# Performance work log

Measured on AMD Instinct MI355X. Metric: run time of the kernel, lower is better.

## Reference

```python
import jax, jax.numpy as jnp
import numpy as np

ALPHA = 0.2  # LeakyReLU negative slope
MASK_VAL = -1e12


def setup_inputs() -> dict:
    key = jax.random.key(0)
    k1, k2, k3, k4 = jax.random.split(key, 4)
    B, N, F_in, F_out = 16, 1024, 128, 64
    inp = jax.random.normal(k1, (B, N, F_in), dtype=jnp.float32)
    adj = jax.random.randint(k2, (B, N, N), 0, 2, dtype=jnp.int32)
    W = jax.random.normal(k3, (F_in, F_out), dtype=jnp.float32) * (1.414 / np.sqrt(F_in))
    a = jax.random.normal(k4, (2 * F_out, 1), dtype=jnp.float32) * (1.414 / np.sqrt(2 * F_out))
    return {"inp": inp, "adj": adj, "W": W, "a": a}


def reference(inp, adj, W, a):
    # inp: [B, N, F_in], adj: [B, N, N], W: [F_in, F_out], a: [2*F_out, 1]
    F_out = W.shape[1]
    h = jnp.einsum('bnf,fo->bno', inp, W)  # [B, N, F_out]
    # e_ij = LeakyReLU(a1 . h_i + a2 . h_j)  (equivalent to concat-then-matmul)
    a1 = a[:F_out, 0]  # [F_out]
    a2 = a[F_out:, 0]  # [F_out]
    e = jax.nn.leaky_relu(
        (h @ a1)[:, :, None] + (h @ a2)[:, None, :], negative_slope=ALPHA
    )  # [B, N, N]
    scores = jnp.where(adj > 0, e, MASK_VAL)
    attention = jax.nn.softmax(scores, axis=-1)  # [B, N, N]
    # dropout with p=0.0 / eval mode -> identity
    h_prime = jnp.einsum('bij,bjo->bio', attention, h)  # [B, N, F_out]
    return jax.nn.elu(h_prime)  # concat=True
```

## Files before the change

kernel.cpp:

```cpp
#include <hip/hip_runtime.h>
#include <cstdint>

#define BB   16
#define NN   1024
#define FIN  128
#define FOUT 64
#define ALPHA_S 0.2f

typedef float    f32x4 __attribute__((ext_vector_type(4)));
typedef _Float16 half8 __attribute__((ext_vector_type(8)));

__device__ inline float wave_sum(float v){
  #pragma unroll
  for (int off = 32; off; off >>= 1) v += __shfl_xor(v, off, 64);
  return v;
}

__global__ __launch_bounds__(256) void k_proj(const float* __restrict__ inp,
                                              const float* __restrict__ W,
                                              const float* __restrict__ a,
                                              _Float16* __restrict__ hT_hi,
                                              _Float16* __restrict__ hT_lo,
                                              float* __restrict__ s1,
                                              float* __restrict__ s2){
  __shared__ float inp_s[32 * FIN];
  const int t = threadIdx.x;
  const int w = t >> 6, f = t & 63;
  const int row0 = blockIdx.x * 32;

  {
    const float4* gsrc = (const float4*)(inp + (size_t)row0 * FIN);
    float4* ldst = (float4*)inp_s;
    #pragma unroll
    for (int i = 0; i < 4; ++i) ldst[i * 256 + t] = gsrc[i * 256 + t];
  }
  __syncthreads();

  float acc[8] = {0.f,0.f,0.f,0.f,0.f,0.f,0.f,0.f};
  const float* ls = inp_s + w * 8 * FIN;
  #pragma unroll 4
  for (int k4 = 0; k4 < 32; ++k4){
    float w0 = W[(k4 * 4 + 0) * FOUT + f];
    float w1 = W[(k4 * 4 + 1) * FOUT + f];
    float w2 = W[(k4 * 4 + 2) * FOUT + f];
    float w3 = W[(k4 * 4 + 3) * FOUT + f];
    #pragma unroll
    for (int r = 0; r < 8; ++r){
      float4 iv = *(const float4*)(ls + r * FIN + k4 * 4);
      acc[r] = fmaf(iv.x, w0, acc[r]);
      acc[r] = fmaf(iv.y, w1, acc[r]);
      acc[r] = fmaf(iv.z, w2, acc[r]);
      acc[r] = fmaf(iv.w, w3, acc[r]);
    }
  }

  const float a1f = a[f], a2f = a[FOUT + f];
  const int rbase = row0 + w * 8;
  #pragma unroll
  for (int r = 0; r < 8; ++r){
    float v1 = wave_sum(acc[r] * a1f);
    float v2 = wave_sum(acc[r] * a2f);
    if (f == 0){ s1[rbase + r] = v1; s2[rbase + r] = v2; }
  }

  half8 hv, lv;
  #pragma unroll
  for (int r = 0; r < 8; ++r){
    _Float16 hi = (_Float16)acc[r];
    hv[r] = hi;
    lv[r] = (_Float16)(acc[r] - (float)hi);
  }
  const int b  = row0 >> 10;
  const int j0 = (row0 & 1023) + w * 8;
  size_t idx = (size_t)b * 65536 + (size_t)(j0 >> 5) * 2048
             + (size_t)f * 32 + (size_t)(j0 & 31);
  *(half8*)(hT_hi + idx) = hv;
  *(half8*)(hT_lo + idx) = lv;
}

__global__ __launch_bounds__(256) void k_attn(const int* __restrict__ adj,
                                              const _Float16* __restrict__ hT_hi,
                                              const _Float16* __restrict__ hT_lo,
                                              const float* __restrict__ s1,
                                              const float* __restrict__ s2,
                                              float* __restrict__ out){
  __shared__ float s2_s[NN];
  __shared__ float redmax[4][16];
  __shared__ float redl[4][16];
  __shared__ float csum[4][1088];

  const int t = threadIdx.x;
  const int w = t >> 6, lane = t & 63;
  const int m16 = lane & 15, g = lane >> 4;
  const int b  = blockIdx.x >> 6;
  const int i0 = (blockIdx.x & 63) * 16;
  const int jb = w * 256;

  *(float4*)&s2_s[jb + lane * 4] = *(const float4*)(s2 + b * NN + jb + lane * 4);

  const float s1i = s1[b * NN + i0 + m16];

  const int* arow = adj + ((size_t)(b * NN + i0 + m16)) * NN + jb + g * 8;
  int4 A0[8], A1[8];
  #pragma unroll
  for (int kk = 0; kk < 8; ++kk){
    A0[kk] = *(const int4*)(arow + kk * 32);
    A1[kk] = *(const int4*)(arow + kk * 32 + 4);
  }

  unsigned mask_lo = 0u, mask_hi = 0u;
  float mxp = -3.0e38f;
  #pragma unroll
  for (int kk = 0; kk < 8; ++kk){
    float4 sA = *(const float4*)&s2_s[jb + kk * 32 + g * 8];
    float4 sB = *(const float4*)&s2_s[jb + kk * 32 + g * 8 + 4];
    unsigned bits = 0u;
    bits |= (A0[kk].x > 0) ? 1u   : 0u;  mxp = fmaxf(mxp, A0[kk].x > 0 ? sA.x : -3.0e38f);
    bits |= (A0[kk].y > 0) ? 2u   : 0u;  mxp = fmaxf(mxp, A0[kk].y > 0 ? sA.y : -3.0e38f);
    bits |= (A0[kk].z > 0) ? 4u   : 0u;  mxp = fmaxf(mxp, A0[kk].z > 0 ? sA.z : -3.0e38f);
    bits |= (A0[kk].w > 0) ? 8u   : 0u;  mxp = fmaxf(mxp, A0[kk].w > 0 ? sA.w : -3.0e38f);
    bits |= (A1[kk].x > 0) ? 16u  : 0u;  mxp = fmaxf(mxp, A1[kk].x > 0 ? sB.x : -3.0e38f);
    bits |= (A1[kk].y > 0) ? 32u  : 0u;  mxp = fmaxf(mxp, A1[kk].y > 0 ? sB.y : -3.0e38f);
    bits |= (A1[kk].z > 0) ? 64u  : 0u;  mxp = fmaxf(mxp, A1[kk].z > 0 ? sB.z : -3.0e38f);
    bits |= (A1[kk].w > 0) ? 128u : 0u;  mxp = fmaxf(mxp, A1[kk].w > 0 ? sB.w : -3.0e38f);
    if (kk < 4) mask_lo |= bits << (kk * 8);
    else        mask_hi |= bits << ((kk - 4) * 8);
  }

  mxp = fmaxf(mxp, __shfl_xor(mxp, 16, 64));
  mxp = fmaxf(mxp, __shfl_xor(mxp, 32, 64));
  if (g == 0) redmax[w][m16] = mxp;
  __syncthreads();
  float mxg = fmaxf(fmaxf(redmax[0][m16], redmax[1][m16]),
                    fmaxf(redmax[2][m16], redmax[3][m16]));
  const bool empty = (mxg < -1.0e38f);
  const float xm = s1i + mxg;
  const float mrow = fmaxf(xm, ALPHA_S * xm);

  f32x4 acc0 = {0,0,0,0}, acc1 = {0,0,0,0}, acc2 = {0,0,0,0}, acc3 = {0,0,0,0};
  float psum = 0.f;
  const size_t bbase = (size_t)b * 65536 + (size_t)(w * 8) * 2048
                     + (size_t)m16 * 32 + (size_t)g * 8;
  const _Float16* bhp = hT_hi + bbase;
  const _Float16* blp = hT_lo + bbase;

  #pragma unroll
  for (int kk = 0; kk < 8; ++kk){
    float4 sA = *(const float4*)&s2_s[jb + kk * 32 + g * 8];
    float4 sB = *(const float4*)&s2_s[jb + kk * 32 + g * 8 + 4];
    const unsigned bits = (kk < 4) ? (mask_lo >> (kk * 8)) : (mask_hi >> ((kk - 4) * 8));
    const float sv[8] = {sA.x, sA.y, sA.z, sA.w, sB.x, sB.y, sB.z, sB.w};
    half8 af;
    #pragma unroll
    for (int u = 0; u < 8; ++u){
      float x = s1i + sv[u];
      float e = fmaxf(x, ALPHA_S * x);
      float p = __expf(e - mrow);
      p = ((bits >> u) & 1u) ? p : 0.0f;
      p = empty ? 1.0f : p;
      psum += p;
      af[u] = (_Float16)p;
    }
    half8 b0h = *(const half8*)(bhp + kk * 2048);
    half8 b1h = *(const half8*)(bhp + kk * 2048 + 512);
    half8 b2h = *(const half8*)(bhp + kk * 2048 + 1024);
    half8 b3h = *(const half8*)(bhp + kk * 2048 + 1536);
    half8 b0l = *(const half8*)(blp + kk * 2048);
    half8 b1l = *(const half8*)(blp + kk * 2048 + 512);
    half8 b2l = *(const half8*)(blp + kk * 2048 + 1024);
    half8 b3l = *(const half8*)(blp + kk * 2048 + 1536);
    acc0 = __builtin_amdgcn_mfma_f32_16x16x32_f16(af, b0h, acc0, 0, 0, 0);
    acc0 = __builtin_amdgcn_mfma_f32_16x16x32_f16(af, b0l, acc0, 0, 0, 0);
    acc1 = __builtin_amdgcn_mfma_f32_16x16x32_f16(af, b1h, acc1, 0, 0, 0);
    acc1 = __builtin_amdgcn_mfma_f32_16x16x32_f16(af, b1l, acc1, 0, 0, 0);
    acc2 = __builtin_amdgcn_mfma_f32_16x16x32_f16(af, b2h, acc2, 0, 0, 0);
    acc2 = __builtin_amdgcn_mfma_f32_16x16x32_f16(af, b2l, acc2, 0, 0, 0);
    acc3 = __builtin_amdgcn_mfma_f32_16x16x32_f16(af, b3h, acc3, 0, 0, 0);
    acc3 = __builtin_amdgcn_mfma_f32_16x16x32_f16(af, b3l, acc3, 0, 0, 0);
  }

  psum += __shfl_xor(psum, 16, 64);
  psum += __shfl_xor(psum, 32, 64);
  if (g == 0) redl[w][m16] = psum;

  #pragma unroll
  for (int q = 0; q < 4; ++q){
    csum[w][(g * 4 + q) * 68 +  0 + m16] = acc0[q];
    csum[w][(g * 4 + q) * 68 + 16 + m16] = acc1[q];
    csum[w][(g * 4 + q) * 68 + 32 + m16] = acc2[q];
    csum[w][(g * 4 + q) * 68 + 48 + m16] = acc3[q];
  }
  __syncthreads();

  const int r  = t >> 4;
  const int c4 = (t & 15) * 4;
  f32x4 sum = *(const f32x4*)&csum[0][r * 68 + c4];
  sum += *(const f32x4*)&csum[1][r * 68 + c4];
  sum += *(const f32x4*)&csum[2][r * 68 + c4];
  sum += *(const f32x4*)&csum[3][r * 68 + c4];
  const float linv = 1.0f / (redl[0][r] + redl[1][r] + redl[2][r] + redl[3][r]);
  f32x4 o;
  #pragma unroll
  for (int u = 0; u < 4; ++u){
    float v = sum[u] * linv;
    o[u] = v > 0.f ? v : __expf(v) - 1.0f;
  }
  *(f32x4*)(out + ((size_t)(b * NN + i0 + r)) * FOUT + c4) = o;
}

extern "C" void kernel_launch(void* const* d_in, const int* in_sizes, int n_in,
                              void* d_out, int out_size, void* d_ws, size_t ws_size,
                              hipStream_t stream) {
  (void)in_sizes; (void)n_in; (void)out_size; (void)ws_size;
  const float* inp = (const float*)d_in[0];
  const int*   adj = (const int*)d_in[1];
  const float* W   = (const float*)d_in[2];
  const float* a   = (const float*)d_in[3];
  float* outp = (float*)d_out;

  _Float16* hT_hi = (_Float16*)d_ws;
  _Float16* hT_lo = hT_hi + (size_t)BB * 65536;
  float* s1 = (float*)(hT_lo + (size_t)BB * 65536);
  float* s2 = s1 + BB * NN;

  k_proj<<<BB * NN / 32, 256, 0, stream>>>(inp, W, a, hT_hi, hT_lo, s1, s2);
  k_attn<<<BB * (NN / 16), 256, 0, stream>>>(adj, hT_hi, hT_lo, s1, s2, outp);
}
```

Baseline: 128.1 us.

## Use split-fp16 MFMA in projection and drop lo-part of h in attention

```diff
diff --git a/kernel.cpp b/kernel.cpp
--- a/kernel.cpp
+++ b/kernel.cpp
@@ -9,78 +9,90 @@
 
 typedef float    f32x4 __attribute__((ext_vector_type(4)));
 typedef _Float16 half8 __attribute__((ext_vector_type(8)));
-
-__device__ inline float wave_sum(float v){
-  #pragma unroll
-  for (int off = 32; off; off >>= 1) v += __shfl_xor(v, off, 64);
-  return v;
-}
+typedef _Float16 half4 __attribute__((ext_vector_type(4)));
 
 __global__ __launch_bounds__(256) void k_proj(const float* __restrict__ inp,
                                               const float* __restrict__ W,
                                               const float* __restrict__ a,
-                                              _Float16* __restrict__ hT_hi,
-                                              _Float16* __restrict__ hT_lo,
+                                              _Float16* __restrict__ hT,
                                               float* __restrict__ s1,
                                               float* __restrict__ s2){
-  __shared__ float inp_s[32 * FIN];
+  __shared__ float red1[4][16];
+  __shared__ float red2[4][16];
   const int t = threadIdx.x;
-  const int w = t >> 6, f = t & 63;
-  const int row0 = blockIdx.x * 32;
-
-  {
-    const float4* gsrc = (const float4*)(inp + (size_t)row0 * FIN);
-    float4* ldst = (float4*)inp_s;
-    #pragma unroll
-    for (int i = 0; i < 4; ++i) ldst[i * 256 + t] = gsrc[i * 256 + t];
-  }
+  const int w = t >> 6, lane = t & 63;
+  const int m16 = lane & 15, g = lane >> 4;
+  const int i0 = blockIdx.x * 16;
+  const int b  = i0 >> 10;
+  const int j0 = i0 & 1023;
+  const int c0 = w * 16;
+
+  const float* arow = inp + (size_t)(i0 + m16) * FIN;
+
+  f32x4 acc = {0.f, 0.f, 0.f, 0.f};
+  #pragma unroll
+  for (int kk = 0; kk < 4; ++kk){
+    const int kbase = kk * 32 + g * 8;
+    float4 av0 = *(const float4*)(arow + kbase);
+    float4 av1 = *(const float4*)(arow + kbase + 4);
+    const float av[8] = {av0.x, av0.y, av0.z, av0.w, av1.x, av1.y, av1.z, av1.w};
+    half8 ah, al;
+    #pragma unroll
+    for (int j = 0; j < 8; ++j){
+      _Float16 h = (_Float16)av[j];
+      ah[j] = h;
+      al[j] = (_Float16)(av[j] - (float)h);
+    }
+    half8 bh, bl;
+    #pragma unroll
+    for (int j = 0; j < 8; ++j){
+      float wv = W[(kbase + j) * FOUT + c0 + m16];
+      _Float16 h = (_Float16)wv;
+      bh[j] = h;
+      bl[j] = (_Float16)(wv - (float)h);
+    }
+    acc = __builtin_amdgcn_mfma_f32_16x16x32_f16(ah, bh, acc, 0, 0, 0);
+    acc = __builtin_amdgcn_mfma_f32_16x16x32_f16(ah, bl, acc, 0, 0, 0);
+    acc = __builtin_amdgcn_mfma_f32_16x16x32_f16(al, bh, acc, 0, 0, 0);
+  }
+
+  const float a1c = a[c0 + m16];
+  const float a2c = a[FOUT + c0 + m16];
+  f32x4 p1, p2;
+  #pragma unroll
+  for (int q = 0; q < 4; ++q){ p1[q] = acc[q] * a1c; p2[q] = acc[q] * a2c; }
+  #pragma unroll
+  for (int off = 1; off < 16; off <<= 1){
+    #pragma unroll
+    for (int q = 0; q < 4; ++q){
+      p1[q] += __shfl_xor(p1[q], off, 64);
+      p2[q] += __shfl_xor(p2[q], off, 64);
+    }
+  }
+  if (m16 == 0){
+    #pragma unroll
+    for (int q = 0; q < 4; ++q){
+      red1[w][g * 4 + q] = p1[q];
+      red2[w][g * 4 + q] = p2[q];
+    }
+  }
+
+  half4 hv;
+  #pragma unroll
+  for (int q = 0; q < 4; ++q) hv[q] = (_Float16)acc[q];
+  size_t idx = (size_t)b * 65536 + (size_t)(j0 >> 5) * 2048
+             + (size_t)(c0 + m16) * 32 + (size_t)(j0 & 31) + (size_t)g * 4;
+  *(half4*)(hT + idx) = hv;
+
   __syncthreads();
-
-  float acc[8] = {0.f,0.f,0.f,0.f,0.f,0.f,0.f,0.f};
-  const float* ls = inp_s + w * 8 * FIN;
-  #pragma unroll 4
-  for (int k4 = 0; k4 < 32; ++k4){
-    float w0 = W[(k4 * 4 + 0) * FOUT + f];
-    float w1 = W[(k4 * 4 + 1) * FOUT + f];
-    float w2 = W[(k4 * 4 + 2) * FOUT + f];
-    float w3 = W[(k4 * 4 + 3) * FOUT + f];
-    #pragma unroll
-    for (int r = 0; r < 8; ++r){
-      float4 iv = *(const float4*)(ls + r * FIN + k4 * 4);
-      acc[r] = fmaf(iv.x, w0, acc[r]);
-      acc[r] = fmaf(iv.y, w1, acc[r]);
-      acc[r] = fmaf(iv.z, w2, acc[r]);
-      acc[r] = fmaf(iv.w, w3, acc[r]);
-    }
-  }
-
-  const float a1f = a[f], a2f = a[FOUT + f];
-  const int rbase = row0 + w * 8;
-  #pragma unroll
-  for (int r = 0; r < 8; ++r){
-    float v1 = wave_sum(acc[r] * a1f);
-    float v2 = wave_sum(acc[r] * a2f);
-    if (f == 0){ s1[rbase + r] = v1; s2[rbase + r] = v2; }
-  }
-
-  half8 hv, lv;
-  #pragma unroll
-  for (int r = 0; r < 8; ++r){
-    _Float16 hi = (_Float16)acc[r];
-    hv[r] = hi;
-    lv[r] = (_Float16)(acc[r] - (float)hi);
-  }
-  const int b  = row0 >> 10;
-  const int j0 = (row0 & 1023) + w * 8;
-  size_t idx = (size_t)b * 65536 + (size_t)(j0 >> 5) * 2048
-             + (size_t)f * 32 + (size_t)(j0 & 31);
-  *(half8*)(hT_hi + idx) = hv;
-  *(half8*)(hT_lo + idx) = lv;
+  if (t < 16){
+    s1[i0 + t] = red1[0][t] + red1[1][t] + red1[2][t] + red1[3][t];
+    s2[i0 + t] = red2[0][t] + red2[1][t] + red2[2][t] + red2[3][t];
+  }
 }
 
 __global__ __launch_bounds__(256) void k_attn(const int* __restrict__ adj,
-                                              const _Float16* __restrict__ hT_hi,
-                                              const _Float16* __restrict__ hT_lo,
+                                              const _Float16* __restrict__ hT,
                                               const float* __restrict__ s1,
                                               const float* __restrict__ s2,
                                               float* __restrict__ out){
@@ -141,8 +153,7 @@
   float psum = 0.f;
   const size_t bbase = (size_t)b * 65536 + (size_t)(w * 8) * 2048
                      + (size_t)m16 * 32 + (size_t)g * 8;
-  const _Float16* bhp = hT_hi + bbase;
-  const _Float16* blp = hT_lo + bbase;
+  const _Float16* bhp = hT + bbase;
 
   #pragma unroll
   for (int kk = 0; kk < 8; ++kk){
@@ -158,25 +169,17 @@
       float p = __expf(e - mrow);
       p = ((bits >> u) & 1u) ? p : 0.0f;
       p = empty ? 1.0f : p;
-      psum += p;
       af[u] = (_Float16)p;
-    }
-    half8 b0h = *(const half8*)(bhp + kk * 2048);
-    half8 b1h = *(const half8*)(bhp + kk * 2048 + 512);
-    half8 b2h = *(const half8*)(bhp + kk * 2048 + 1024);
-    half8 b3h = *(const half8*)(bhp + kk * 2048 + 1536);
-    half8 b0l = *(const half8*)(blp + kk * 2048);
-    half8 b1l = *(const half8*)(blp + kk * 2048 + 512);
-    half8 b2l = *(const half8*)(blp + kk * 2048 + 1024);
-    half8 b3l = *(const half8*)(blp + kk * 2048 + 1536);
-    acc0 = __builtin_amdgcn_mfma_f32_16x16x32_f16(af, b0h, acc0, 0, 0, 0);
-    acc0 = __builtin_amdgcn_mfma_f32_16x16x32_f16(af, b0l, acc0, 0, 0, 0);
-    acc1 = __builtin_amdgcn_mfma_f32_16x16x32_f16(af, b1h, acc1, 0, 0, 0);
-    acc1 = __builtin_amdgcn_mfma_f32_16x16x32_f16(af, b1l, acc1, 0, 0, 0);
-    acc2 = __builtin_amdgcn_mfma_f32_16x16x32_f16(af, b2h, acc2, 0, 0, 0);
-    acc2 = __builtin_amdgcn_mfma_f32_16x16x32_f16(af, b2l, acc2, 0, 0, 0);
-    acc3 = __builtin_amdgcn_mfma_f32_16x16x32_f16(af, b3h, acc3, 0, 0, 0);
-    acc3 = __builtin_amdgcn_mfma_f32_16x16x32_f16(af, b3l, acc3, 0, 0, 0);
+      psum += (float)af[u];
+    }
+    half8 b0 = *(const half8*)(bhp + kk * 2048);
+    half8 b1 = *(const half8*)(bhp + kk * 2048 + 512);
+    half8 b2 = *(const half8*)(bhp + kk * 2048 + 1024);
+    half8 b3 = *(const half8*)(bhp + kk * 2048 + 1536);
+    acc0 = __builtin_amdgcn_mfma_f32_16x16x32_f16(af, b0, acc0, 0, 0, 0);
+    acc1 = __builtin_amdgcn_mfma_f32_16x16x32_f16(af, b1, acc1, 0, 0, 0);
+    acc2 = __builtin_amdgcn_mfma_f32_16x16x32_f16(af, b2, acc2, 0, 0, 0);
+    acc3 = __builtin_amdgcn_mfma_f32_16x16x32_f16(af, b3, acc3, 0, 0, 0);
   }
 
   psum += __shfl_xor(psum, 16, 64);
@@ -218,11 +221,10 @@
   const float* a   = (const float*)d_in[3];
   float* outp = (float*)d_out;
 
-  _Float16* hT_hi = (_Float16*)d_ws;
-  _Float16* hT_lo = hT_hi + (size_t)BB * 65536;
-  float* s1 = (float*)(hT_lo + (size_t)BB * 65536);
+  _Float16* hT = (_Float16*)d_ws;
+  float* s1 = (float*)(hT + (size_t)BB * 65536);
   float* s2 = s1 + BB * NN;
 
-  k_proj<<<BB * NN / 32, 256, 0, stream>>>(inp, W, a, hT_hi, hT_lo, s1, s2);
-  k_attn<<<BB * (NN / 16), 256, 0, stream>>>(adj, hT_hi, hT_lo, s1, s2, outp);
+  k_proj<<<BB * NN / 16, 256, 0, stream>>>(inp, W, a, hT, s1, s2);
+  k_attn<<<BB * (NN / 16), 256, 0, stream>>>(adj, hT, s1, s2, outp);
 }
```

Result: faster. 114.6 us (-10.5%).
